# Kernel tuning notes

Measured on AMD Instinct MI355X. Metric: run time of the kernel, lower is better.

Reference implementation:

```python
import jax, jax.numpy as jnp
import numpy as np

N_BALLS = 256
BATCH = 128
N_STEPS = 100
MAX_EVENTS = 5
WORLD_W = 10.0
WORLD_H = 10.0
RADIUS = 0.1
HID = 64
DT = 0.05
INF = jnp.float32(1e30)

_II_np, _JJ_np = np.triu_indices(N_BALLS, 1)
_II = jnp.asarray(_II_np)
_JJ = jnp.asarray(_JJ_np)
# wall order: left, right, bottom, top (normals point into the box)
_WN = jnp.array([[1.0, 0.0], [-1.0, 0.0], [0.0, 1.0], [0.0, -1.0]], dtype=jnp.float32)
_WP = jnp.array([0.0, -WORLD_W, 0.0, -WORLD_H], dtype=jnp.float32)


def setup_inputs():
    key = jax.random.key(0)
    ks = jax.random.split(key, 6)
    pos = jax.random.uniform(ks[0], (BATCH, N_BALLS, 2), minval=0.5, maxval=9.5)
    vel = jax.random.normal(ks[1], (BATCH, N_BALLS, 2))
    state = jnp.concatenate([pos, vel], axis=-1)  # [B, N, 4]
    radii = jnp.full((N_BALLS,), RADIUS, dtype=jnp.float32)
    sc = 0.1
    W1 = jax.random.normal(ks[2], (HID, 2)) * sc
    b1 = jnp.zeros((HID,), jnp.float32)
    W2 = jax.random.normal(ks[3], (HID, HID)) * sc
    b2 = jnp.zeros((HID,), jnp.float32)
    W3 = jax.random.normal(ks[4], (1, HID)) * sc
    b3 = jnp.zeros((1,), jnp.float32)
    return {"state": state, "radii": radii, "W1": W1, "b1": b1, "W2": W2,
            "b2": b2, "W3": W3, "b3": b3, "dt": DT, "n_steps": N_STEPS}


def _detect(pos, vel, radii):
    # pos, vel: [N,2]; vectorized replacement of the Python O(N^2) loop.
    diff = pos[_JJ] - pos[_II]                       # [P,2]
    dist = jnp.linalg.norm(diff, axis=-1)            # [P]
    gap_b = dist - (radii[_II] + radii[_JJ])
    nhat = diff / (dist + 1e-8)[:, None]
    app_b = jnp.sum((vel[_JJ] - vel[_II]) * nhat, axis=-1)
    gb = jnp.where(app_b < 0, gap_b, INF)            # only approaching pairs
    r = radii
    gw = jnp.stack([pos[:, 0] - r, WORLD_W - pos[:, 0] - r,
                    pos[:, 1] - r, WORLD_H - pos[:, 1] - r], axis=-1)  # [N,4]
    vw = jnp.stack([vel[:, 0] < 0, vel[:, 0] > 0,
                    vel[:, 1] < 0, vel[:, 1] > 0], axis=-1)
    gw = jnp.where(vw, gw, INF)
    allg = jnp.concatenate([gb, gw.reshape(-1)])
    k = jnp.argmin(allg)
    P = gb.shape[0]
    is_ball = k < P
    gap = allg[k]
    bi = jnp.where(is_ball, k, 0)
    i_b, j_b = _II[bi], _JJ[bi]
    kw = jnp.where(is_ball, 0, k - P)
    i_w, wid = kw // 4, kw % 4
    return gap, is_ball, i_b, j_b, i_w, wid


def _apply_jump(s, i, j, W1, b1, W2, b2, W3, b3):
    pos, vel = s[..., :2], s[..., 2:]
    diff = pos[:, j] - pos[:, i]                               # [B,2]
    dist = jnp.maximum(jnp.linalg.norm(diff, axis=-1, keepdims=True), 1e-8)
    nhat = diff / dist
    app = jnp.sum((vel[:, j] - vel[:, i]) * nhat, axis=-1, keepdims=True)
    h = jnp.concatenate([dist, app], axis=-1)                  # [B,2]
    h = jax.nn.silu(h @ W1.T + b1)
    h = jax.nn.silu(h @ W2.T + b2)
    imp = (h @ W3.T + b3) * nhat                               # [B,2]
    vel_new = vel.at[:, i].add(imp).at[:, j].add(-imp)
    return jnp.concatenate([pos, vel_new], axis=-1)


def _apply_wall(s, i, wn, wp, r):
    pos, vel = s[..., :2], s[..., 2:]
    v, p = vel[:, i], pos[:, i]
    vn = jnp.sum(v * wn, axis=-1, keepdims=True)
    vel_new = vel.at[:, i].set(v - 2.0 * vn * wn)
    pn = jnp.sum(p * wn, axis=-1, keepdims=True)
    pen = jnp.maximum(wp + r - pn, 0.0)
    pos_new = pos.at[:, i].set(p + pen * wn)
    return jnp.concatenate([pos_new, vel_new], axis=-1)


def _rollout(state, radii, W1, b1, W2, b2, W3, b3, dt, n_steps):
    dt = jnp.float32(dt)

    def event_body(_, carry):
        curr, t_c, t_e, done = carry
        pos0, vel0 = curr[0, :, :2], curr[0, :, 2:]
        gap, is_ball, i_b, j_b, i_w, wid = _detect(pos0, vel0, radii)
        no_event = gap > 0.05
        n = pos0[j_b] - pos0[i_b]
        app_ball = -jnp.sum((vel0[j_b] - vel0[i_b]) * n / jnp.linalg.norm(n))
        app_wall = jnp.abs(jnp.max(vel0[i_w]))
        app = jnp.where(is_ball, app_ball, app_wall)
        t_ev = t_c + gap / jnp.maximum(app, 1e-6)
        # ZeroFlow is constant velocity -> dopri5 integrate is exact linear drift
        dte = jnp.where(t_ev > t_c + 1e-10, t_ev - t_c, 0.0)

        def apply_map(s):
            jm = _apply_jump(s, i_b, j_b, W1, b1, W2, b2, W3, b3)
            wm = _apply_wall(s, i_w, _WN[wid], _WP[wid], radii[i_w])
            return jnp.where(is_ball, jm, wm)

        state_a = apply_map(curr)                       # gap <= 0: jump now
        integ = curr.at[..., :2].add(curr[..., 2:] * dte)
        state_b = apply_map(integ)                      # 0 < gap: drift then jump
        act = (~done) & (~no_event)
        case_a = act & (gap <= 0)
        case_b = act & (gap > 0) & (app > 1e-6) & (t_ev < t_e)
        new_done = done | no_event | (act & (gap > 0) & ((app <= 1e-6) | (t_ev >= t_e)))
        new_curr = jnp.where(case_a, state_a, jnp.where(case_b, state_b, curr))
        new_t_c = jnp.where(case_b, t_ev, t_c)
        return new_curr, new_t_c, t_e, new_done

    def step(curr, step_idx):
        t_s = step_idx.astype(jnp.float32) * dt
        t_e = t_s + dt
        curr, t_c, _, _ = jax.lax.fori_loop(
            0, MAX_EVENTS, event_body, (curr, t_s, t_e, jnp.bool_(False)))
        dte = jnp.where(t_e > t_c + 1e-10, t_e - t_c, 0.0)
        curr = curr.at[..., :2].add(curr[..., 2:] * dte)
        return curr, curr

    _, traj = jax.lax.scan(step, state, jnp.arange(n_steps))
    return jnp.concatenate([state[None], traj], axis=0)   # [n_steps+1, B, N, 4]


def reference(state, radii, W1, b1, W2, b2, W3, b3, dt, n_steps):
    return _rollout(state, radii, W1, b1, W2, b2, W3, b3, dt, n_steps)
```

## Files before the change

### kernel.cpp

```cpp
#include <hip/hip_runtime.h>
#include <stdint.h>

#define NB 256
#define NBATCH 128
#define HID 64
#define MAXEV 5
#define MAXSTEPS 256
#define NT 43
#define NTILES 946
#define W2S 65
#define CAND_MAX 6144
#define T_MAX 1536
#define CMARGIN 1.5f
#define TMARG 0.8f
#define NTHR 512
#define D2GATE 0.0626f

typedef unsigned long long u64;

__device__ __forceinline__ float bf2f(unsigned short u) {
    return __uint_as_float(((unsigned)u) << 16);
}
__device__ __forceinline__ unsigned short f2bf(float f) {
    unsigned u = __float_as_uint(f);
    u += 0x7FFFu + ((u >> 16) & 1u);
    return (unsigned short)(u >> 16);
}
__device__ __forceinline__ float rdin(const void* p, int idx, int bf) {
    return bf ? bf2f(((const unsigned short*)p)[idx]) : ((const float*)p)[idx];
}
__device__ __forceinline__ float silu_f(float x) {
    float s = __fdiv_rn(1.0f, __fadd_rn(1.0f, expf(-x)));
    return __fmul_rn(x, s);
}
__device__ __forceinline__ void lds_fence() {
    __builtin_amdgcn_wave_barrier();
    __threadfence_block();
    __builtin_amdgcn_wave_barrier();
}
__device__ __forceinline__ u64 shfl_down_u64(u64 v, int off) {
    unsigned lo = (unsigned)v, hi = (unsigned)(v >> 32);
    lo = __shfl_down(lo, off);
    hi = __shfl_down(hi, off);
    return (((u64)hi) << 32) | lo;
}
__device__ __forceinline__ unsigned fmap(float g) {
    unsigned u = __float_as_uint(g);
    unsigned m = (unsigned)(((int)u) >> 31) | 0x80000000u;
    return u ^ m;
}
__device__ __forceinline__ float funmap(unsigned sb) {
    unsigned u = (sb & 0x80000000u) ? (sb ^ 0x80000000u) : ~sb;
    return __uint_as_float(u);
}

__device__ __forceinline__ void append_agg(unsigned* list, int* counter, int cap, unsigned val) {
    u64 m = __ballot(1);
    int lane = (int)(threadIdx.x & 63);
    int ldr = (int)__builtin_ctzll(m);
    int pfx = (int)__builtin_popcountll(m & ((1ull << lane) - 1ull));
    int base = 0;
    if (lane == ldr) base = atomicAdd(counter, (int)__builtin_popcountll(m));
    base = __builtin_amdgcn_readfirstlane(base);
    int idx = base + pfx;
    if (idx < cap) list[idx] = val;
}

__device__ __forceinline__ u64 ball_key(const float4* ps, int i, int j,
                                        float dx, float dy, float d2,
                                        unsigned id, float rsum) {
    float4 A = ps[i], B = ps[j];
    float p1 = __fmul_rn(__fsub_rn(B.z, A.z), dx);
    float p2 = __fmul_rn(__fsub_rn(B.w, A.w), dy);
    float dot = __fadd_rn(p1, p2);
    float mag = __fadd_rn(fabsf(p1), fabsf(p2));
    bool appr;
    if (fabsf(dot) < __fmul_rn(1e-5f, mag)) {
        float dist = __fsqrt_rn(d2);
        float den = __fadd_rn(dist, 1e-8f);
        float ab = __fadd_rn(__fmul_rn(__fsub_rn(B.z, A.z), __fdiv_rn(dx, den)),
                             __fmul_rn(__fsub_rn(B.w, A.w), __fdiv_rn(dy, den)));
        appr = ab < 0.0f;
    } else {
        appr = dot < 0.0f;
    }
    if (!appr) return ~0ull;
    float gap = __fsub_rn(__fsqrt_rn(d2), rsum);
    return (((u64)fmap(gap)) << 17) | id;
}

__device__ __forceinline__ void scan_list(const unsigned* src, int n,
                                          const float2* pos2, const float4* ps0,
                                          float rsum, float th2T,
                                          bool buildT, unsigned* cand2, int* candN2,
                                          u64& kC, int tid) {
    unsigned idq[8];
    #pragma unroll
    for (int q = 0; q < 8; q++) {
        int c = tid + q * NTHR;
        idq[q] = (c < n) ? src[c] : 0u;
    }
    float2 Aq[8], Bq[8];
    #pragma unroll
    for (int q = 0; q < 8; q++) {
        Aq[q] = pos2[idq[q] >> 8];
        Bq[q] = pos2[idq[q] & 255u];
    }
    #pragma unroll
    for (int q = 0; q < 8; q++) {
        float dx = __fsub_rn(Bq[q].x, Aq[q].x), dy = __fsub_rn(Bq[q].y, Aq[q].y);
        float d2 = __fadd_rn(__fmul_rn(dx, dx), __fmul_rn(dy, dy));
        bool live = (tid + q * NTHR) < n;
        if (buildT) {
            if (live && d2 < th2T) append_agg(cand2, candN2, T_MAX, idq[q]);
        }
        if (live && d2 < D2GATE) {
            u64 key = ball_key(ps0, (int)(idq[q] >> 8), (int)(idq[q] & 255u),
                               dx, dy, d2, idq[q], rsum);
            kC = key < kC ? key : kC;
        }
    }
    for (int c = tid + 8 * NTHR; c < n; c += NTHR) {
        unsigned id = src[c];
        float2 A = pos2[id >> 8], B = pos2[id & 255u];
        float dx = __fsub_rn(B.x, A.x), dy = __fsub_rn(B.y, A.y);
        float d2 = __fadd_rn(__fmul_rn(dx, dx), __fmul_rn(dy, dy));
        if (buildT && d2 < th2T) append_agg(cand2, candN2, T_MAX, id);
        if (d2 < D2GATE) {
            u64 key = ball_key(ps0, (int)(id >> 8), (int)(id & 255u), dx, dy, d2, id, rsum);
            kC = key < kC ? key : kC;
        }
    }
}

__device__ __forceinline__ void scan_full(const float2* pos2, const float4* ps0, float rsum,
                                          int i0a, int j0a, int i0b, int j0b,
                                          bool apB, float th2B, unsigned* cand, int* candN,
                                          bool apT, float th2T, unsigned* cand2, int* candN2,
                                          u64& kC) {
    #pragma unroll
    for (int tt = 0; tt < 2; tt++) {
        int I0 = tt ? i0b : i0a;
        int J0 = tt ? j0b : j0a;
        if (I0 < 0) continue;
        float2 Pi[6], Pj[6];
        #pragma unroll
        for (int a = 0; a < 6; a++) {
            int ii = I0 + a; ii = ii < NB ? ii : NB - 1;
            int jj = J0 + a; jj = jj < NB ? jj : NB - 1;
            Pi[a] = pos2[ii]; Pj[a] = pos2[jj];
        }
        #pragma unroll
        for (int a = 0; a < 6; a++) {
            int i = I0 + a;
            #pragma unroll
            for (int bb = 0; bb < 6; bb++) {
                int j = J0 + bb;
                bool ok = (i < NB) && (j < NB) && (j > i);
                float dx = __fsub_rn(Pj[bb].x, Pi[a].x);
                float dy = __fsub_rn(Pj[bb].y, Pi[a].y);
                float d2 = __fadd_rn(__fmul_rn(dx, dx), __fmul_rn(dy, dy));
                unsigned id = (unsigned)((i << 8) | j);
                if (apB && ok && d2 < th2B) append_agg(cand, candN, CAND_MAX, id);
                if (apT && ok && d2 < th2T) append_agg(cand2, candN2, T_MAX, id);
                if (ok && d2 < D2GATE) {
                    u64 key = ball_key(ps0, i, j, dx, dy, d2, id, rsum);
                    kC = key < kC ? key : kC;
                }
            }
        }
    }
}

__device__ void load_weights(float* w1, float* b1s, float* w2, float* b2s, float* w3, float* b3s,
                             const void* W1, const void* B1, const void* W2, const void* B2,
                             const void* W3, const void* B3, int bf, int tid, int nthr) {
    for (int k = tid; k < HID * 2; k += nthr) w1[k] = rdin(W1, k, bf);
    for (int k = tid; k < HID; k += nthr) {
        b1s[k] = rdin(B1, k, bf);
        b2s[k] = rdin(B2, k, bf);
        w3[k]  = rdin(W3, k, bf);
    }
    for (int k = tid; k < HID * HID; k += nthr) {
        int m = k >> 6, c = k & 63;
        w2[m * W2S + c] = rdin(W2, k, bf);
    }
    if (tid == 0) b3s[0] = rdin(B3, 0, bf);
}

__global__ void sniff_kernel(const unsigned short* st, int* ws) {
    __shared__ int ev;
    if (threadIdx.x == 0) ev = 0;
    __syncthreads();
    unsigned short u = st[threadIdx.x];
    int e = (u >> 7) & 0xFF;
    if (e >= 0x85) atomicOr(&ev, 1);
    __syncthreads();
    if (threadIdx.x == 0) ws[0] = ev ? 0 : 1;
}

__global__ void row0_kernel(const void* in, void* out, const int* ws) {
    int idx = blockIdx.x * blockDim.x + threadIdx.x;
    if (ws[0]) ((unsigned short*)out)[idx] = ((const unsigned short*)in)[idx];
    else       ((float*)out)[idx] = ((const float*)in)[idx];
}

__global__ __launch_bounds__(NTHR, 1) void sim_kernel(
    const void* in_state, const void* in_rad,
    const void* inW1, const void* inB1, const void* inW2, const void* inB2,
    const void* inW3, const void* inB3, const void* in_dt, const int* in_nsteps,
    void* out, const int* ws) {
    __shared__ float4 ps0[NB];
    __shared__ float4 psb[NB];
    __shared__ float2 pos2[NB];
    __shared__ float w1[HID * 2], b1s[HID], w2[HID * W2S], b2s[HID], w3s[HID], b3s[1];
    __shared__ float sc0[132], scb[132];
    __shared__ u64 redK[8];
    __shared__ float redF[4];
    __shared__ unsigned cand[CAND_MAX];
    __shared__ unsigned cand2[T_MAX];
    __shared__ int candN, candN2;
    __shared__ int pubF;
    __shared__ int rebF;

    int tid = threadIdx.x;
    int b = blockIdx.x;
    int bf = ws[0];

    if (tid < NB) {
        int base0 = tid * 4;
        float4 P;
        P.x = rdin(in_state, base0 + 0, bf);
        P.y = rdin(in_state, base0 + 1, bf);
        P.z = rdin(in_state, base0 + 2, bf);
        P.w = rdin(in_state, base0 + 3, bf);
        ps0[tid] = P;
        float2 p2v; p2v.x = P.x; p2v.y = P.y;
        pos2[tid] = p2v;
        int baseb = (b * NB + tid) * 4;
        float4 Q;
        Q.x = rdin(in_state, baseb + 0, bf);
        Q.y = rdin(in_state, baseb + 1, bf);
        Q.z = rdin(in_state, baseb + 2, bf);
        Q.w = rdin(in_state, baseb + 3, bf);
        psb[tid] = Q;
        float m2 = P.z * P.z + P.w * P.w;
        #pragma unroll
        for (int off = 32; off; off >>= 1) m2 = fmaxf(m2, __shfl_down(m2, off));
        if ((tid & 63) == 0) redF[tid >> 6] = m2;
    }
    load_weights(w1, b1s, w2, b2s, w3s, b3s, inW1, inB1, inW2, inB2, inW3, inB3, bf, tid, NTHR);
    if (tid == 0) { candN = 0; candN2 = 0; pubF = 0; rebF = 1; }

    float dtv = rdin(in_dt, 0, bf);
    int NS = in_nsteps[0]; if (NS > MAXSTEPS) NS = MAXSTEPS; if (NS < 0) NS = 0;
    float rad0 = rdin(in_rad, 0, bf);
    float rsum = __fadd_rn(rad0, rad0);

    int i0a = -1, j0a = 0, i0b = -1, j0b = 0;
    {
        int T = tid;
        if (T < NTILES) {
            int rem = T, r = 0;
            while (rem >= NT - r) { rem -= NT - r; r++; }
            i0a = r * 6; j0a = (r + rem) * 6;
        }
        T = tid + NTHR;
        if (T < NTILES) {
            int rem = T, r = 0;
            while (rem >= NT - r) { rem -= NT - r; r++; }
            i0b = r * 6; j0b = (r + rem) * 6;
        }
    }
    __syncthreads();

    float thB = __fadd_rn(__fadd_rn(rsum, 0.05f), CMARGIN);
    float th2B = __fmul_rn(thB, thB);
    float thT = __fadd_rn(__fsqrt_rn(D2GATE), TMARG);
    float th2T = __fmul_rn(thT, thT);

    int nc = 0, ncT = 0;
    bool candOvf = false, tOvf = false;
    float used = 1e30f, vcap = 0.0f, U0 = 0.0f;

    for (int s = 0; s < NS; s++) {
        int rebuild = rebF;
        float t_s = __fmul_rn((float)s, dtv);
        float t_e = __fadd_rn(t_s, dtv);
        float t_c = t_s;
        if (tid < 64) {
            if (rebuild) {
                vcap = sqrtf(fmaxf(fmaxf(redF[0], redF[1]), fmaxf(redF[2], redF[3])));
                used = 0.0f;
            }
            U0 = used;
            used = __fadd_rn(used, __fmul_rn(__fmul_rn(2.0f, dtv), vcap));
        }

        for (int e = 0; e < MAXEV; e++) {
            u64 kC = ~0ull;
            bool buildT = (e == 0);
            int mode;
            if (e == 0) mode = rebuild ? 2 : 1;
            else { int pf = pubF; mode = (pf & 1) ? 2 : ((pf & 2) ? 1 : 0); }
            if (mode == 2) {
                scan_full(pos2, ps0, rsum, i0a, j0a, i0b, j0b,
                          buildT, th2B, cand, &candN,
                          buildT, th2T, cand2, &candN2, kC);
            } else if (mode == 1) {
                scan_list(cand, nc, pos2, ps0, rsum, th2T, buildT, cand2, &candN2, kC, tid);
            } else {
                scan_list(cand2, ncT, pos2, ps0, rsum, th2T, false, cand2, &candN2, kC, tid);
            }
            {
                int ball = tid & 255, wsel = tid >> 8;
                float4 P = ps0[ball];
                #pragma unroll
                for (int q = 0; q < 2; q++) {
                    int w = wsel * 2 + q;
                    float g; bool valid;
                    if (w == 0)      { g = __fsub_rn(P.x, rad0); valid = P.z < 0.0f; }
                    else if (w == 1) { g = __fsub_rn(__fsub_rn(10.0f, P.x), rad0); valid = P.z > 0.0f; }
                    else if (w == 2) { g = __fsub_rn(P.y, rad0); valid = P.w < 0.0f; }
                    else             { g = __fsub_rn(__fsub_rn(10.0f, P.y), rad0); valid = P.w > 0.0f; }
                    if (valid) {
                        u64 key = (((u64)fmap(g)) << 17) | 0x10000u | (unsigned)(ball * 4 + w);
                        kC = key < kC ? key : kC;
                    }
                }
            }
            #pragma unroll
            for (int off = 32; off; off >>= 1) {
                u64 o = shfl_down_u64(kC, off);
                kC = o < kC ? o : kC;
            }
            if ((tid & 63) == 0) redK[tid >> 6] = kC;
            __syncthreads();

            if (e == 0) {
                if (rebuild) {
                    int ct = candN;
                    candOvf = ct > CAND_MAX;
                    nc = candOvf ? CAND_MAX : ct;
                }
                int ct2 = candN2;
                tOvf = ct2 > T_MAX;
                ncT = tOvf ? T_MAX : ct2;
            }

            float g_nx = 0, g_ny = 0, g_dist = 0, g_app = 0;
            float4 gA, gB;
            int code = 0; float dteB = 0.0f; float tcn = t_c;
            int ei = 0, ejw = 0;
            {
                u64 m = redK[0];
                #pragma unroll
                for (int q = 1; q < 8; q++) m = redK[q] < m ? redK[q] : m;
                if (m != ~0ull) {
                    bool is_ball = ((m >> 16) & 1ull) == 0;
                    unsigned id = (unsigned)(m & 0xFFFFull);
                    float gap = funmap((unsigned)(m >> 17));
                    int pi = (int)(id >> 8), pj = (int)(id & 255u);
                    int wb = (int)(id >> 2), ww = (int)(id & 3u);
                    ei = is_ball ? pi : wb;
                    ejw = is_ball ? pj : ww;
                    if (!(gap > 0.05f)) {
                        float app;
                        if (is_ball) {
                            float4 A = ps0[pi], B = ps0[pj];
                            float dx = __fsub_rn(B.x, A.x), dy = __fsub_rn(B.y, A.y);
                            float nrm = __fsqrt_rn(__fadd_rn(__fmul_rn(dx, dx), __fmul_rn(dy, dy)));
                            float dvx = __fsub_rn(B.z, A.z), dvy = __fsub_rn(B.w, A.w);
                            app = -__fadd_rn(__fdiv_rn(__fmul_rn(dvx, dx), nrm),
                                             __fdiv_rn(__fmul_rn(dvy, dy), nrm));
                        } else {
                            float4 Wb = ps0[wb];
                            app = fabsf(fmaxf(Wb.z, Wb.w));
                        }
                        float t_ev = __fadd_rn(t_c, __fdiv_rn(gap, fmaxf(app, 1e-6f)));
                        if (gap <= 0.0f) {
                            code = is_ball ? 1 : 3;
                        } else if (app > 1e-6f && t_ev < t_e) {
                            code = is_ball ? 2 : 4;
                            dteB = (t_ev > __fadd_rn(t_c, 1e-10f)) ? __fsub_rn(t_ev, t_c) : 0.0f;
                            tcn = t_ev;
                        }
                    }
                }
                if (code != 0 && code <= 2) {
                    float4 A = ps0[ei], B = ps0[ejw];
                    if (code == 2) {
                        A.x = __fadd_rn(A.x, __fmul_rn(A.z, dteB));
                        A.y = __fadd_rn(A.y, __fmul_rn(A.w, dteB));
                        B.x = __fadd_rn(B.x, __fmul_rn(B.z, dteB));
                        B.y = __fadd_rn(B.y, __fmul_rn(B.w, dteB));
                    }
                    gA = A; gB = B;
                    float dx = __fsub_rn(B.x, A.x), dy = __fsub_rn(B.y, A.y);
                    float nrm = __fsqrt_rn(__fadd_rn(__fmul_rn(dx, dx), __fmul_rn(dy, dy)));
                    float dist = fmaxf(nrm, 1e-8f);
                    g_nx = __fdiv_rn(dx, dist); g_ny = __fdiv_rn(dy, dist);
                    g_dist = dist;
                    float dvx = __fsub_rn(B.z, A.z), dvy = __fsub_rn(B.w, A.w);
                    g_app = __fadd_rn(__fmul_rn(dvx, g_nx), __fmul_rn(dvy, g_ny));
                }
            }
            if (code == 0) break;
            t_c = tcn;
            bool integ = (code == 2) || (code == 4);
            __syncthreads();

            if (code <= 2) {
                if (tid < 64) {
                    float a = __fadd_rn(__fadd_rn(__fmul_rn(g_dist, w1[2 * tid]),
                                                  __fmul_rn(g_app, w1[2 * tid + 1])), b1s[tid]);
                    sc0[4 + tid] = silu_f(a);
                    lds_fence();
                    float acc = 0.0f;
                    const float* row = &w2[tid * W2S];
                    #pragma unroll 8
                    for (int k = 0; k < HID; k++) acc = __fadd_rn(acc, __fmul_rn(sc0[4 + k], row[k]));
                    acc = __fadd_rn(acc, b2s[tid]);
                    sc0[68 + tid] = silu_f(acc);
                    lds_fence();
                    float acc3 = 0.0f;
                    #pragma unroll 8
                    for (int k = 0; k < HID; k++)
                        acc3 = __fadd_rn(acc3, __fmul_rn(sc0[68 + k], w3s[k]));
                    float impv = __fadd_rn(acc3, b3s[0]);
                    float ix = __fmul_rn(impv, g_nx), iy = __fmul_rn(impv, g_ny);
                    float nAz = __fadd_rn(gA.z, ix),  nAw = __fadd_rn(gA.w, iy);
                    float nBz = __fadd_rn(gB.z, -ix), nBw = __fadd_rn(gB.w, -iy);
                    if (tid == 0) {
                        float4 outA; outA.x = gA.x; outA.y = gA.y; outA.z = nAz; outA.w = nAw;
                        float4 outB; outB.x = gB.x; outB.y = gB.y; outB.z = nBz; outB.w = nBw;
                        ps0[ei] = outA; ps0[ejw] = outB;
                        float2 pa; pa.x = gA.x; pa.y = gA.y; pos2[ei] = pa;
                        float2 pb; pb.x = gB.x; pb.y = gB.y; pos2[ejw] = pb;
                    }
                    float s1 = sqrtf(nAz * nAz + nAw * nAw);
                    float s2 = sqrtf(nBz * nBz + nBw * nBw);
                    float nv = fmaxf(s1, s2);
                    used = __fadd_rn(used, __fmul_rn(__fmul_rn(2.0f, dtv),
                                                     fmaxf(__fsub_rn(nv, vcap), 0.0f)));
                    vcap = fmaxf(vcap, nv);
                    int nf  = (candOvf || (__fadd_rn(used, 1e-3f) > CMARGIN)) ? 1 : 0;
                    int nft = (tOvf || (__fadd_rn(__fsub_rn(used, U0), 1e-3f) > TMARG)) ? 1 : 0;
                    if (tid == 0) pubF = nf | (nft << 1);
                } else if (tid < 128) {
                    int lane = tid - 64;
                    float4 A = psb[ei], B = psb[ejw];
                    if (integ) {
                        A.x = __fadd_rn(A.x, __fmul_rn(A.z, dteB));
                        A.y = __fadd_rn(A.y, __fmul_rn(A.w, dteB));
                        B.x = __fadd_rn(B.x, __fmul_rn(B.z, dteB));
                        B.y = __fadd_rn(B.y, __fmul_rn(B.w, dteB));
                    }
                    float dx = __fsub_rn(B.x, A.x), dy = __fsub_rn(B.y, A.y);
                    float nrm = __fsqrt_rn(__fadd_rn(__fmul_rn(dx, dx), __fmul_rn(dy, dy)));
                    float dist = fmaxf(nrm, 1e-8f);
                    float nx = __fdiv_rn(dx, dist), ny = __fdiv_rn(dy, dist);
                    float dvx = __fsub_rn(B.z, A.z), dvy = __fsub_rn(B.w, A.w);
                    float app2 = __fadd_rn(__fmul_rn(dvx, nx), __fmul_rn(dvy, ny));
                    float a = __fadd_rn(__fadd_rn(__fmul_rn(dist, w1[2 * lane]),
                                                  __fmul_rn(app2, w1[2 * lane + 1])), b1s[lane]);
                    scb[4 + lane] = silu_f(a);
                    lds_fence();
                    float acc = 0.0f;
                    const float* row = &w2[lane * W2S];
                    #pragma unroll 8
                    for (int k = 0; k < HID; k++) acc = __fadd_rn(acc, __fmul_rn(scb[4 + k], row[k]));
                    acc = __fadd_rn(acc, b2s[lane]);
                    scb[68 + lane] = silu_f(acc);
                    lds_fence();
                    float acc3 = 0.0f;
                    #pragma unroll 8
                    for (int k = 0; k < HID; k++)
                        acc3 = __fadd_rn(acc3, __fmul_rn(scb[68 + k], w3s[k]));
                    float impv = __fadd_rn(acc3, b3s[0]);
                    if (lane == 0) {
                        float ix = __fmul_rn(impv, nx), iy = __fmul_rn(impv, ny);
                        float4 outA; outA.x = A.x; outA.y = A.y;
                        outA.z = __fadd_rn(A.z, ix);  outA.w = __fadd_rn(A.w, iy);
                        float4 outB; outB.x = B.x; outB.y = B.y;
                        outB.z = __fadd_rn(B.z, -ix); outB.w = __fadd_rn(B.w, -iy);
                        psb[ei] = outA; psb[ejw] = outB;
                    }
                } else if (tid < 384) {
                    int t = tid - 128;
                    if (integ && t != ei && t != ejw) {
                        float4 P = ps0[t];
                        P.x = __fadd_rn(P.x, __fmul_rn(P.z, dteB));
                        P.y = __fadd_rn(P.y, __fmul_rn(P.w, dteB));
                        ps0[t] = P;
                        float2 pp; pp.x = P.x; pp.y = P.y; pos2[t] = pp;
                    }
                } else {
                    #pragma unroll
                    for (int q = 0; q < 2; q++) {
                        int t = (tid - 384) + q * 128;
                        if (integ && t != ei && t != ejw) {
                            float4 Q = psb[t];
                            Q.x = __fadd_rn(Q.x, __fmul_rn(Q.z, dteB));
                            Q.y = __fadd_rn(Q.y, __fmul_rn(Q.w, dteB));
                            psb[t] = Q;
                        }
                    }
                }
                __syncthreads();
            } else {
                const float wnx[4] = {1.f, -1.f, 0.f, 0.f};
                const float wny[4] = {0.f, 0.f, 1.f, -1.f};
                const float wpv[4] = {0.f, -10.f, 0.f, -10.f};
                int w = ejw;
                if (tid < 64) {
                    float4 P = ps0[ei];
                    if (integ) {
                        P.x = __fadd_rn(P.x, __fmul_rn(P.z, dteB));
                        P.y = __fadd_rn(P.y, __fmul_rn(P.w, dteB));
                    }
                    float vn = __fadd_rn(__fmul_rn(P.z, wnx[w]), __fmul_rn(P.w, wny[w]));
                    float t2 = __fmul_rn(2.0f, vn);
                    float nvx = __fsub_rn(P.z, __fmul_rn(t2, wnx[w]));
                    float nvy = __fsub_rn(P.w, __fmul_rn(t2, wny[w]));
                    float pn = __fadd_rn(__fmul_rn(P.x, wnx[w]), __fmul_rn(P.y, wny[w]));
                    float pen = fmaxf(__fsub_rn(__fadd_rn(wpv[w], rad0), pn), 0.0f);
                    float4 nP;
                    nP.x = __fadd_rn(P.x, __fmul_rn(pen, wnx[w]));
                    nP.y = __fadd_rn(P.y, __fmul_rn(pen, wny[w]));
                    nP.z = nvx; nP.w = nvy;
                    used = __fadd_rn(used, pen);
                    int nf  = (candOvf || (__fadd_rn(used, 1e-3f) > CMARGIN)) ? 1 : 0;
                    int nft = (tOvf || (__fadd_rn(__fsub_rn(used, U0), 1e-3f) > TMARG)) ? 1 : 0;
                    if (tid == 0) {
                        ps0[ei] = nP;
                        float2 pp; pp.x = nP.x; pp.y = nP.y; pos2[ei] = pp;
                        pubF = nf | (nft << 1);
                    }
                } else if (tid < 128) {
                    if (tid == 64) {
                        float4 P = psb[ei];
                        if (integ) {
                            P.x = __fadd_rn(P.x, __fmul_rn(P.z, dteB));
                            P.y = __fadd_rn(P.y, __fmul_rn(P.w, dteB));
                        }
                        float vn = __fadd_rn(__fmul_rn(P.z, wnx[w]), __fmul_rn(P.w, wny[w]));
                        float t2 = __fmul_rn(2.0f, vn);
                        float nvx = __fsub_rn(P.z, __fmul_rn(t2, wnx[w]));
                        float nvy = __fsub_rn(P.w, __fmul_rn(t2, wny[w]));
                        float pn = __fadd_rn(__fmul_rn(P.x, wnx[w]), __fmul_rn(P.y, wny[w]));
                        float pen = fmaxf(__fsub_rn(__fadd_rn(wpv[w], rad0), pn), 0.0f);
                        float4 nP;
                        nP.x = __fadd_rn(P.x, __fmul_rn(pen, wnx[w]));
                        nP.y = __fadd_rn(P.y, __fmul_rn(pen, wny[w]));
                        nP.z = nvx; nP.w = nvy;
                        psb[ei] = nP;
                    }
                } else if (tid < 384) {
                    int t = tid - 128;
                    if (integ && t != ei) {
                        float4 P = ps0[t];
                        P.x = __fadd_rn(P.x, __fmul_rn(P.z, dteB));
                        P.y = __fadd_rn(P.y, __fmul_rn(P.w, dteB));
                        ps0[t] = P;
                        float2 pp; pp.x = P.x; pp.y = P.y; pos2[t] = pp;
                    }
                } else {
                    #pragma unroll
                    for (int q = 0; q < 2; q++) {
                        int t = (tid - 384) + q * 128;
                        if (integ && t != ei) {
                            float4 Q = psb[t];
                            Q.x = __fadd_rn(Q.x, __fmul_rn(Q.z, dteB));
                            Q.y = __fadd_rn(Q.y, __fmul_rn(Q.w, dteB));
                            psb[t] = Q;
                        }
                    }
                }
                __syncthreads();
            }
        }

        float fd = (t_e > __fadd_rn(t_c, 1e-10f)) ? __fsub_rn(t_e, t_c) : 0.0f;
        if (tid < NB) {
            float4 P = ps0[tid];
            P.x = __fadd_rn(P.x, __fmul_rn(P.z, fd));
            P.y = __fadd_rn(P.y, __fmul_rn(P.w, fd));
            ps0[tid] = P;
            float2 pp; pp.x = P.x; pp.y = P.y; pos2[tid] = pp;
            float m2 = P.z * P.z + P.w * P.w;
            #pragma unroll
            for (int off = 32; off; off >>= 1) m2 = fmaxf(m2, __shfl_down(m2, off));
            if ((tid & 63) == 0) redF[tid >> 6] = m2;
            if (tid == 0) {
                candN = 0; candN2 = 0;
                float usedNext = __fadd_rn(used, __fmul_rn(__fmul_rn(2.0f, dtv), vcap));
                rebF = (candOvf || (__fadd_rn(usedNext, 1e-3f) > CMARGIN)) ? 1 : 0;
            }
        } else {
            int t = tid - NB;
            float4 Q = psb[t];
            Q.x = __fadd_rn(Q.x, __fmul_rn(Q.z, fd));
            Q.y = __fadd_rn(Q.y, __fmul_rn(Q.w, fd));
            psb[t] = Q;
            long long base = ((long long)(s + 1) * NBATCH + b) * (NB * 4);
            if (bf) {
                ushort4 v;
                v.x = f2bf(Q.x); v.y = f2bf(Q.y); v.z = f2bf(Q.z); v.w = f2bf(Q.w);
                ((ushort4*)((unsigned short*)out + base))[t] = v;
            } else {
                ((float4*)((float*)out + base))[t] = Q;
            }
        }
        __syncthreads();
    }
}

extern "C" void kernel_launch(void* const* d_in, const int* in_sizes, int n_in,
                              void* d_out, int out_size, void* d_ws, size_t ws_size,
                              hipStream_t stream) {
    int* ws = (int*)d_ws;
    sniff_kernel<<<1, 256, 0, stream>>>((const unsigned short*)d_in[0], ws);
    row0_kernel<<<(NBATCH * NB * 4) / 256, 256, 0, stream>>>(d_in[0], d_out, ws);
    sim_kernel<<<NBATCH, NTHR, 0, stream>>>(
        d_in[0], d_in[1], d_in[2], d_in[3], d_in[4], d_in[5], d_in[6], d_in[7],
        d_in[8], (const int*)d_in[9], d_out, ws);
}
```

Baseline: 3.995 ms.

## Double-buffer ball state to drop a barrier per event and remove secondary candidate list

```diff
diff --git a/kernel.cpp b/kernel.cpp
--- a/kernel.cpp
+++ b/kernel.cpp
@@ -10,9 +10,7 @@
 #define NTILES 946
 #define W2S 65
 #define CAND_MAX 6144
-#define T_MAX 1536
 #define CMARGIN 1.5f
-#define TMARG 0.8f
 #define NTHR 512
 #define D2GATE 0.0626f
 
@@ -90,10 +88,8 @@
 }
 
 __device__ __forceinline__ void scan_list(const unsigned* src, int n,
-                                          const float2* pos2, const float4* ps0,
-                                          float rsum, float th2T,
-                                          bool buildT, unsigned* cand2, int* candN2,
-                                          u64& kC, int tid) {
+                                          const float2* pos2c, const float4* ps0c,
+                                          float rsum, u64& kC, int tid) {
     unsigned idq[8];
     #pragma unroll
     for (int q = 0; q < 8; q++) {
@@ -103,40 +99,35 @@
     float2 Aq[8], Bq[8];
     #pragma unroll
     for (int q = 0; q < 8; q++) {
-        Aq[q] = pos2[idq[q] >> 8];
-        Bq[q] = pos2[idq[q] & 255u];
+        Aq[q] = pos2c[idq[q] >> 8];
+        Bq[q] = pos2c[idq[q] & 255u];
     }
     #pragma unroll
     for (int q = 0; q < 8; q++) {
         float dx = __fsub_rn(Bq[q].x, Aq[q].x), dy = __fsub_rn(Bq[q].y, Aq[q].y);
         float d2 = __fadd_rn(__fmul_rn(dx, dx), __fmul_rn(dy, dy));
         bool live = (tid + q * NTHR) < n;
-        if (buildT) {
-            if (live && d2 < th2T) append_agg(cand2, candN2, T_MAX, idq[q]);
-        }
         if (live && d2 < D2GATE) {
-            u64 key = ball_key(ps0, (int)(idq[q] >> 8), (int)(idq[q] & 255u),
+            u64 key = ball_key(ps0c, (int)(idq[q] >> 8), (int)(idq[q] & 255u),
                                dx, dy, d2, idq[q], rsum);
             kC = key < kC ? key : kC;
         }
     }
     for (int c = tid + 8 * NTHR; c < n; c += NTHR) {
         unsigned id = src[c];
-        float2 A = pos2[id >> 8], B = pos2[id & 255u];
+        float2 A = pos2c[id >> 8], B = pos2c[id & 255u];
         float dx = __fsub_rn(B.x, A.x), dy = __fsub_rn(B.y, A.y);
         float d2 = __fadd_rn(__fmul_rn(dx, dx), __fmul_rn(dy, dy));
-        if (buildT && d2 < th2T) append_agg(cand2, candN2, T_MAX, id);
         if (d2 < D2GATE) {
-            u64 key = ball_key(ps0, (int)(id >> 8), (int)(id & 255u), dx, dy, d2, id, rsum);
+            u64 key = ball_key(ps0c, (int)(id >> 8), (int)(id & 255u), dx, dy, d2, id, rsum);
             kC = key < kC ? key : kC;
         }
     }
 }
 
-__device__ __forceinline__ void scan_full(const float2* pos2, const float4* ps0, float rsum,
+__device__ __forceinline__ void scan_full(const float2* pos2c, const float4* ps0c, float rsum,
                                           int i0a, int j0a, int i0b, int j0b,
                                           bool apB, float th2B, unsigned* cand, int* candN,
-                                          bool apT, float th2T, unsigned* cand2, int* candN2,
                                           u64& kC) {
     #pragma unroll
     for (int tt = 0; tt < 2; tt++) {
@@ -148,7 +139,7 @@
         for (int a = 0; a < 6; a++) {
             int ii = I0 + a; ii = ii < NB ? ii : NB - 1;
             int jj = J0 + a; jj = jj < NB ? jj : NB - 1;
-            Pi[a] = pos2[ii]; Pj[a] = pos2[jj];
+            Pi[a] = pos2c[ii]; Pj[a] = pos2c[jj];
         }
         #pragma unroll
         for (int a = 0; a < 6; a++) {
@@ -162,9 +153,8 @@
                 float d2 = __fadd_rn(__fmul_rn(dx, dx), __fmul_rn(dy, dy));
                 unsigned id = (unsigned)((i << 8) | j);
                 if (apB && ok && d2 < th2B) append_agg(cand, candN, CAND_MAX, id);
-                if (apT && ok && d2 < th2T) append_agg(cand2, candN2, T_MAX, id);
                 if (ok && d2 < D2GATE) {
-                    u64 key = ball_key(ps0, i, j, dx, dy, d2, id, rsum);
+                    u64 key = ball_key(ps0c, i, j, dx, dy, d2, id, rsum);
                     kC = key < kC ? key : kC;
                 }
             }
@@ -210,16 +200,15 @@
     const void* inW1, const void* inB1, const void* inW2, const void* inB2,
     const void* inW3, const void* inB3, const void* in_dt, const int* in_nsteps,
     void* out, const int* ws) {
-    __shared__ float4 ps0[NB];
-    __shared__ float4 psb[NB];
-    __shared__ float2 pos2[NB];
+    __shared__ float4 ps0[2][NB];
+    __shared__ float4 psb[2][NB];
+    __shared__ float2 pos2[2][NB];
     __shared__ float w1[HID * 2], b1s[HID], w2[HID * W2S], b2s[HID], w3s[HID], b3s[1];
     __shared__ float sc0[132], scb[132];
     __shared__ u64 redK[8];
     __shared__ float redF[4];
     __shared__ unsigned cand[CAND_MAX];
-    __shared__ unsigned cand2[T_MAX];
-    __shared__ int candN, candN2;
+    __shared__ int candN;
     __shared__ int pubF;
     __shared__ int rebF;
 
@@ -234,23 +223,23 @@
         P.y = rdin(in_state, base0 + 1, bf);
         P.z = rdin(in_state, base0 + 2, bf);
         P.w = rdin(in_state, base0 + 3, bf);
-        ps0[tid] = P;
+        ps0[0][tid] = P;
         float2 p2v; p2v.x = P.x; p2v.y = P.y;
-        pos2[tid] = p2v;
+        pos2[0][tid] = p2v;
         int baseb = (b * NB + tid) * 4;
         float4 Q;
         Q.x = rdin(in_state, baseb + 0, bf);
         Q.y = rdin(in_state, baseb + 1, bf);
         Q.z = rdin(in_state, baseb + 2, bf);
         Q.w = rdin(in_state, baseb + 3, bf);
-        psb[tid] = Q;
+        psb[0][tid] = Q;
         float m2 = P.z * P.z + P.w * P.w;
         #pragma unroll
         for (int off = 32; off; off >>= 1) m2 = fmaxf(m2, __shfl_down(m2, off));
         if ((tid & 63) == 0) redF[tid >> 6] = m2;
     }
     load_weights(w1, b1s, w2, b2s, w3s, b3s, inW1, inB1, inW2, inB2, inW3, inB3, bf, tid, NTHR);
-    if (tid == 0) { candN = 0; candN2 = 0; pubF = 0; rebF = 1; }
+    if (tid == 0) { candN = 0; pubF = 0; rebF = 1; }
 
     float dtv = rdin(in_dt, 0, bf);
     int NS = in_nsteps[0]; if (NS > MAXSTEPS) NS = MAXSTEPS; if (NS < 0) NS = 0;
@@ -276,12 +265,11 @@
 
     float thB = __fadd_rn(__fadd_rn(rsum, 0.05f), CMARGIN);
     float th2B = __fmul_rn(thB, thB);
-    float thT = __fadd_rn(__fsqrt_rn(D2GATE), TMARG);
-    float th2T = __fmul_rn(thT, thT);
-
-    int nc = 0, ncT = 0;
-    bool candOvf = false, tOvf = false;
-    float used = 1e30f, vcap = 0.0f, U0 = 0.0f;
+
+    int p = 0;
+    int nc = 0;
+    bool candOvf = false;
+    float used = 1e30f, vcap = 0.0f;
 
     for (int s = 0; s < NS; s++) {
         int rebuild = rebF;
@@ -293,28 +281,31 @@
                 vcap = sqrtf(fmaxf(fmaxf(redF[0], redF[1]), fmaxf(redF[2], redF[3])));
                 used = 0.0f;
             }
-            U0 = used;
             used = __fadd_rn(used, __fmul_rn(__fmul_rn(2.0f, dtv), vcap));
         }
 
         for (int e = 0; e < MAXEV; e++) {
+            const float4* ps0c = ps0[p];
+            const float2* pos2c = pos2[p];
+            const float4* psbc = psb[p];
+            float4* ps0n = ps0[p ^ 1];
+            float2* pos2n = pos2[p ^ 1];
+            float4* psbn = psb[p ^ 1];
+
             u64 kC = ~0ull;
-            bool buildT = (e == 0);
             int mode;
             if (e == 0) mode = rebuild ? 2 : 1;
-            else { int pf = pubF; mode = (pf & 1) ? 2 : ((pf & 2) ? 1 : 0); }
+            else        mode = pubF ? 2 : 1;
             if (mode == 2) {
-                scan_full(pos2, ps0, rsum, i0a, j0a, i0b, j0b,
-                          buildT, th2B, cand, &candN,
-                          buildT, th2T, cand2, &candN2, kC);
-            } else if (mode == 1) {
-                scan_list(cand, nc, pos2, ps0, rsum, th2T, buildT, cand2, &candN2, kC, tid);
+                bool apB = (e == 0);
+                scan_full(pos2c, ps0c, rsum, i0a, j0a, i0b, j0b,
+                          apB, th2B, cand, &candN, kC);
             } else {
-                scan_list(cand2, ncT, pos2, ps0, rsum, th2T, false, cand2, &candN2, kC, tid);
+                scan_list(cand, nc, pos2c, ps0c, rsum, kC, tid);
             }
             {
                 int ball = tid & 255, wsel = tid >> 8;
-                float4 P = ps0[ball];
+                float4 P = ps0c[ball];
                 #pragma unroll
                 for (int q = 0; q < 2; q++) {
                     int w = wsel * 2 + q;
@@ -337,15 +328,10 @@
             if ((tid & 63) == 0) redK[tid >> 6] = kC;
             __syncthreads();
 
-            if (e == 0) {
-                if (rebuild) {
-                    int ct = candN;
-                    candOvf = ct > CAND_MAX;
-                    nc = candOvf ? CAND_MAX : ct;
-                }
-                int ct2 = candN2;
-                tOvf = ct2 > T_MAX;
-                ncT = tOvf ? T_MAX : ct2;
+            if (e == 0 && rebuild) {
+                int ct = candN;
+                candOvf = ct > CAND_MAX;
+                nc = candOvf ? CAND_MAX : ct;
             }
 
             float g_nx = 0, g_ny = 0, g_dist = 0, g_app = 0;
@@ -367,14 +353,14 @@
                     if (!(gap > 0.05f)) {
                         float app;
                         if (is_ball) {
-                            float4 A = ps0[pi], B = ps0[pj];
+                            float4 A = ps0c[pi], B = ps0c[pj];
                             float dx = __fsub_rn(B.x, A.x), dy = __fsub_rn(B.y, A.y);
                             float nrm = __fsqrt_rn(__fadd_rn(__fmul_rn(dx, dx), __fmul_rn(dy, dy)));
                             float dvx = __fsub_rn(B.z, A.z), dvy = __fsub_rn(B.w, A.w);
                             app = -__fadd_rn(__fdiv_rn(__fmul_rn(dvx, dx), nrm),
                                              __fdiv_rn(__fmul_rn(dvy, dy), nrm));
                         } else {
-                            float4 Wb = ps0[wb];
+                            float4 Wb = ps0c[wb];
                             app = fabsf(fmaxf(Wb.z, Wb.w));
                         }
                         float t_ev = __fadd_rn(t_c, __fdiv_rn(gap, fmaxf(app, 1e-6f)));
@@ -387,8 +373,8 @@
                         }
                     }
                 }
-                if (code != 0 && code <= 2) {
-                    float4 A = ps0[ei], B = ps0[ejw];
+                if (tid < 64 && code != 0 && code <= 2) {
+                    float4 A = ps0c[ei], B = ps0c[ejw];
                     if (code == 2) {
                         A.x = __fadd_rn(A.x, __fmul_rn(A.z, dteB));
                         A.y = __fadd_rn(A.y, __fmul_rn(A.w, dteB));
@@ -408,7 +394,7 @@
             if (code == 0) break;
             t_c = tcn;
             bool integ = (code == 2) || (code == 4);
-            __syncthreads();
+            int skip2 = (code <= 2) ? ejw : -1;
 
             if (code <= 2) {
                 if (tid < 64) {
@@ -434,9 +420,9 @@
                     if (tid == 0) {
                         float4 outA; outA.x = gA.x; outA.y = gA.y; outA.z = nAz; outA.w = nAw;
                         float4 outB; outB.x = gB.x; outB.y = gB.y; outB.z = nBz; outB.w = nBw;
-                        ps0[ei] = outA; ps0[ejw] = outB;
-                        float2 pa; pa.x = gA.x; pa.y = gA.y; pos2[ei] = pa;
-                        float2 pb; pb.x = gB.x; pb.y = gB.y; pos2[ejw] = pb;
+                        ps0n[ei] = outA; ps0n[ejw] = outB;
+                        float2 pa; pa.x = gA.x; pa.y = gA.y; pos2n[ei] = pa;
+                        float2 pb; pb.x = gB.x; pb.y = gB.y; pos2n[ejw] = pb;
                     }
                     float s1 = sqrtf(nAz * nAz + nAw * nAw);
                     float s2 = sqrtf(nBz * nBz + nBw * nBw);
@@ -444,12 +430,11 @@
                     used = __fadd_rn(used, __fmul_rn(__fmul_rn(2.0f, dtv),
                                                      fmaxf(__fsub_rn(nv, vcap), 0.0f)));
                     vcap = fmaxf(vcap, nv);
-                    int nf  = (candOvf || (__fadd_rn(used, 1e-3f) > CMARGIN)) ? 1 : 0;
-                    int nft = (tOvf || (__fadd_rn(__fsub_rn(used, U0), 1e-3f) > TMARG)) ? 1 : 0;
-                    if (tid == 0) pubF = nf | (nft << 1);
+                    int nf = (candOvf || (__fadd_rn(used, 1e-3f) > CMARGIN)) ? 1 : 0;
+                    if (tid == 0) pubF = nf;
                 } else if (tid < 128) {
                     int lane = tid - 64;
-                    float4 A = psb[ei], B = psb[ejw];
+                    float4 A = psbc[ei], B = psbc[ejw];
                     if (integ) {
                         A.x = __fadd_rn(A.x, __fmul_rn(A.z, dteB));
                         A.y = __fadd_rn(A.y, __fmul_rn(A.w, dteB));
@@ -484,37 +469,16 @@
                         outA.z = __fadd_rn(A.z, ix);  outA.w = __fadd_rn(A.w, iy);
                         float4 outB; outB.x = B.x; outB.y = B.y;
                         outB.z = __fadd_rn(B.z, -ix); outB.w = __fadd_rn(B.w, -iy);
-                        psb[ei] = outA; psb[ejw] = outB;
-                    }
-                } else if (tid < 384) {
-                    int t = tid - 128;
-                    if (integ && t != ei && t != ejw) {
-                        float4 P = ps0[t];
-                        P.x = __fadd_rn(P.x, __fmul_rn(P.z, dteB));
-                        P.y = __fadd_rn(P.y, __fmul_rn(P.w, dteB));
-                        ps0[t] = P;
-                        float2 pp; pp.x = P.x; pp.y = P.y; pos2[t] = pp;
-                    }
-                } else {
-                    #pragma unroll
-                    for (int q = 0; q < 2; q++) {
-                        int t = (tid - 384) + q * 128;
-                        if (integ && t != ei && t != ejw) {
-                            float4 Q = psb[t];
-                            Q.x = __fadd_rn(Q.x, __fmul_rn(Q.z, dteB));
-                            Q.y = __fadd_rn(Q.y, __fmul_rn(Q.w, dteB));
-                            psb[t] = Q;
-                        }
-                    }
-                }
-                __syncthreads();
+                        psbn[ei] = outA; psbn[ejw] = outB;
+                    }
+                }
             } else {
                 const float wnx[4] = {1.f, -1.f, 0.f, 0.f};
                 const float wny[4] = {0.f, 0.f, 1.f, -1.f};
                 const float wpv[4] = {0.f, -10.f, 0.f, -10.f};
                 int w = ejw;
                 if (tid < 64) {
-                    float4 P = ps0[ei];
+                    float4 P = ps0c[ei];
                     if (integ) {
                         P.x = __fadd_rn(P.x, __fmul_rn(P.z, dteB));
                         P.y = __fadd_rn(P.y, __fmul_rn(P.w, dteB));
@@ -530,16 +494,15 @@
                     nP.y = __fadd_rn(P.y, __fmul_rn(pen, wny[w]));
                     nP.z = nvx; nP.w = nvy;
                     used = __fadd_rn(used, pen);
-                    int nf  = (candOvf || (__fadd_rn(used, 1e-3f) > CMARGIN)) ? 1 : 0;
-                    int nft = (tOvf || (__fadd_rn(__fsub_rn(used, U0), 1e-3f) > TMARG)) ? 1 : 0;
+                    int nf = (candOvf || (__fadd_rn(used, 1e-3f) > CMARGIN)) ? 1 : 0;
                     if (tid == 0) {
-                        ps0[ei] = nP;
-                        float2 pp; pp.x = nP.x; pp.y = nP.y; pos2[ei] = pp;
-                        pubF = nf | (nft << 1);
+                        ps0n[ei] = nP;
+                        float2 pp; pp.x = nP.x; pp.y = nP.y; pos2n[ei] = pp;
+                        pubF = nf;
                     }
                 } else if (tid < 128) {
                     if (tid == 64) {
-                        float4 P = psb[ei];
+                        float4 P = psbc[ei];
                         if (integ) {
                             P.x = __fadd_rn(P.x, __fmul_rn(P.z, dteB));
                             P.y = __fadd_rn(P.y, __fmul_rn(P.w, dteB));
@@ -554,55 +517,57 @@
                         nP.x = __fadd_rn(P.x, __fmul_rn(pen, wnx[w]));
                         nP.y = __fadd_rn(P.y, __fmul_rn(pen, wny[w]));
                         nP.z = nvx; nP.w = nvy;
-                        psb[ei] = nP;
-                    }
-                } else if (tid < 384) {
-                    int t = tid - 128;
-                    if (integ && t != ei) {
-                        float4 P = ps0[t];
-                        P.x = __fadd_rn(P.x, __fmul_rn(P.z, dteB));
-                        P.y = __fadd_rn(P.y, __fmul_rn(P.w, dteB));
-                        ps0[t] = P;
-                        float2 pp; pp.x = P.x; pp.y = P.y; pos2[t] = pp;
-                    }
-                } else {
-                    #pragma unroll
-                    for (int q = 0; q < 2; q++) {
-                        int t = (tid - 384) + q * 128;
-                        if (integ && t != ei) {
-                            float4 Q = psb[t];
-                            Q.x = __fadd_rn(Q.x, __fmul_rn(Q.z, dteB));
-                            Q.y = __fadd_rn(Q.y, __fmul_rn(Q.w, dteB));
-                            psb[t] = Q;
-                        }
-                    }
-                }
-                __syncthreads();
-            }
+                        psbn[ei] = nP;
+                    }
+                }
+            }
+            if (tid >= 128 && tid < 384) {
+                int t = tid - 128;
+                if (t != ei && t != skip2) {
+                    float4 P = ps0c[t];
+                    P.x = __fadd_rn(P.x, __fmul_rn(P.z, dteB));
+                    P.y = __fadd_rn(P.y, __fmul_rn(P.w, dteB));
+                    ps0n[t] = P;
+                    float2 pp; pp.x = P.x; pp.y = P.y; pos2n[t] = pp;
+                }
+            } else if (tid >= 384) {
+                #pragma unroll
+                for (int q = 0; q < 2; q++) {
+                    int t = (tid - 384) + q * 128;
+                    if (t != ei && t != skip2) {
+                        float4 Q = psbc[t];
+                        Q.x = __fadd_rn(Q.x, __fmul_rn(Q.z, dteB));
+                        Q.y = __fadd_rn(Q.y, __fmul_rn(Q.w, dteB));
+                        psbn[t] = Q;
+                    }
+                }
+            }
+            __syncthreads();
+            p ^= 1;
         }
 
         float fd = (t_e > __fadd_rn(t_c, 1e-10f)) ? __fsub_rn(t_e, t_c) : 0.0f;
         if (tid < NB) {
-            float4 P = ps0[tid];
+            float4 P = ps0[p][tid];
             P.x = __fadd_rn(P.x, __fmul_rn(P.z, fd));
             P.y = __fadd_rn(P.y, __fmul_rn(P.w, fd));
-            ps0[tid] = P;
-            float2 pp; pp.x = P.x; pp.y = P.y; pos2[tid] = pp;
+            ps0[p ^ 1][tid] = P;
+            float2 pp; pp.x = P.x; pp.y = P.y; pos2[p ^ 1][tid] = pp;
             float m2 = P.z * P.z + P.w * P.w;
             #pragma unroll
             for (int off = 32; off; off >>= 1) m2 = fmaxf(m2, __shfl_down(m2, off));
             if ((tid & 63) == 0) redF[tid >> 6] = m2;
             if (tid == 0) {
-                candN = 0; candN2 = 0;
+                candN = 0;
                 float usedNext = __fadd_rn(used, __fmul_rn(__fmul_rn(2.0f, dtv), vcap));
                 rebF = (candOvf || (__fadd_rn(usedNext, 1e-3f) > CMARGIN)) ? 1 : 0;
             }
         } else {
             int t = tid - NB;
-            float4 Q = psb[t];
+            float4 Q = psb[p][t];
             Q.x = __fadd_rn(Q.x, __fmul_rn(Q.z, fd));
             Q.y = __fadd_rn(Q.y, __fmul_rn(Q.w, fd));
-            psb[t] = Q;
+            psb[p ^ 1][t] = Q;
             long long base = ((long long)(s + 1) * NBATCH + b) * (NB * 4);
             if (bf) {
                 ushort4 v;
@@ -613,6 +578,7 @@
             }
         }
         __syncthreads();
+        p ^= 1;
     }
 }
 
```

Measured after the change: 3.342 ms. -16.4%, faster.
